# Kernel optimization log

Hardware: AMD Instinct MI355X
Metric: run time of the kernel (lower is better)

The kernel has to match this reference:

```python
import jax, jax.numpy as jnp
import numpy as np

LEFT = 16  # attention window size (previous `left` symbols incl. current)


def _make_history(symbols, left):
    """contexts[b, t, j] = symbols[b, t - (left-1-j)] for j in [0,left),
    padded with symbols[b, 0] for out-of-range positions (pad = symbols[:, :1])."""
    B, T = symbols.shape
    # (T, left) gather index matrix
    idx = jnp.arange(T)[:, None] - (left - 1 - jnp.arange(left))[None, :]
    valid = idx >= 0
    idx_c = jnp.clip(idx, 0, T - 1)
    ctx = symbols[:, idx_c]                                   # (B, T, left)
    pad = symbols[:, :1][:, :, None]                          # (B, 1, 1)
    return jnp.where(valid[None, :, :], ctx, pad)             # (B, T, left)


def setup_inputs() -> dict:
    key = jax.random.key(0)
    k1, k2, k3, k4 = jax.random.split(key, 4)
    B, T, V, D = 8, 2048, 256, 512
    symbols = jax.random.randint(k1, (B, T), 0, V, dtype=jnp.int32)
    encodings = jax.random.normal(k2, (B, T, D), dtype=jnp.float32)
    # keras 'uniform' initializer: U(-0.05, 0.05)
    M = jax.random.uniform(k3, (V, D), minval=-0.05, maxval=0.05, dtype=jnp.float32)
    C = jax.random.uniform(k4, (V, D), minval=-0.05, maxval=0.05, dtype=jnp.float32)
    return {"symbols": symbols, "encodings": encodings, "M": M, "C": C}


def reference(symbols, encodings, M, C):
    contexts = _make_history(symbols, LEFT)                   # (B, T, L) int
    Mg = M[contexts]                                          # (B, T, L, D)
    Cg = C[contexts]                                          # (B, T, L, D)
    scores = jnp.einsum('btld,btd->btl', Mg, encodings)       # (B, T, L)
    p = jax.nn.softmax(scores, axis=-1)                       # (B, T, L)
    compressed = jnp.einsum('btl,btld->btd', p, Cg)           # (B, T, D)
    output = jnp.concatenate([compressed, encodings], axis=-1)  # (B, T, 2D)
    return output, p
```

## Files before the change

kernel.cpp:

```cpp
#include <hip/hip_runtime.h>

#define B_ 8
#define T_ 2048
#define V_ 256
#define D_ 512
#define LEFT_ 16
#define TPW 4
#define NR (TPW + LEFT_ - 1)

__device__ __forceinline__ constexpr int rev6(int x) {
    return (((x >> 0) & 1) << 5) | (((x >> 1) & 1) << 4) | (((x >> 2) & 1) << 3) |
           (((x >> 3) & 1) << 2) | (((x >> 4) & 1) << 1) | (((x >> 5) & 1) << 0);
}

__device__ __forceinline__ float dot8(const float4& m0, const float4& m1,
                                      const float4& e0, const float4& e1) {
    return m0.x * e0.x + m0.y * e0.y + m0.z * e0.z + m0.w * e0.w
         + m1.x * e1.x + m1.y * e1.y + m1.z * e1.z + m1.w * e1.w;
}

__global__ __launch_bounds__(256)
void attn_cell_kernel(const int* __restrict__ symbols,
                      const float* __restrict__ encodings,
                      const float* __restrict__ M,
                      const float* __restrict__ C,
                      float* __restrict__ out,
                      float* __restrict__ p_out) {
    const int tid  = threadIdx.x;
    const int lane = tid & 63;
    const int w    = tid >> 6;

    const int blk = blockIdx.x;
    const int b   = blk >> 7;
    const int tb  = (blk & 127) * 16 + w * TPW;
    const int* symrow = symbols + b * T_;
    const size_t rowbase = (size_t)b * T_ + tb;
    const int dof = lane * 8;

    int syms[NR];
    #pragma unroll
    for (int i = 0; i < NR; ++i) {
        int pos = tb - (LEFT_ - 1) + i;
        pos = max(pos, 0);
        syms[i] = symrow[pos];
    }

    float4 e0[TPW], e1[TPW];
    #pragma unroll
    for (int tk = 0; tk < TPW; ++tk) {
        const float* e = encodings + (rowbase + tk) * D_ + dof;
        e0[tk] = *(const float4*)e;
        e1[tk] = *(const float4*)(e + 4);
    }

    float s[64];
    #pragma unroll
    for (int v = 0; v < 64; ++v) s[v] = 0.f;

    #pragma unroll
    for (int i = 0; i < NR; ++i) {
        const float* mr = M + (size_t)syms[i] * D_ + dof;
        const float4 m0 = *(const float4*)mr;
        const float4 m1 = *(const float4*)(mr + 4);
        #pragma unroll
        for (int tk = 0; tk < TPW; ++tk) {
            const int sl = i - tk;
            if (sl >= 0 && sl < 16)
                s[(tk << 4) | sl] += dot8(m0, m1, e0[tk], e1[tk]);
        }
    }

    #pragma unroll
    for (int k = 0; k < 32; ++k) {
        const float lo = s[k], hi = s[k + 32];
        const float sd = (lane & 1) ? lo : hi;
        const float rv = __shfl_xor(sd, 1);
        s[k] = (lane & 1) ? hi + rv : lo + rv;
    }
    #pragma unroll
    for (int k = 0; k < 16; ++k) {
        const float lo = s[k], hi = s[k + 16];
        const float sd = (lane & 2) ? lo : hi;
        const float rv = __shfl_xor(sd, 2);
        s[k] = (lane & 2) ? hi + rv : lo + rv;
    }
    #pragma unroll
    for (int k = 0; k < 8; ++k) {
        const float lo = s[k], hi = s[k + 8];
        const float sd = (lane & 4) ? lo : hi;
        const float rv = __shfl_xor(sd, 4);
        s[k] = (lane & 4) ? hi + rv : lo + rv;
    }
    #pragma unroll
    for (int k = 0; k < 4; ++k) {
        const float lo = s[k], hi = s[k + 4];
        const float sd = (lane & 8) ? lo : hi;
        const float rv = __shfl_xor(sd, 8);
        s[k] = (lane & 8) ? hi + rv : lo + rv;
    }
    #pragma unroll
    for (int k = 0; k < 2; ++k) {
        const float lo = s[k], hi = s[k + 2];
        const float sd = (lane & 16) ? lo : hi;
        const float rv = __shfl_xor(sd, 16);
        s[k] = (lane & 16) ? hi + rv : lo + rv;
    }
    {
        const float lo = s[0], hi = s[1];
        const float sd = (lane & 32) ? lo : hi;
        const float rv = __shfl_xor(sd, 32);
        s[0] = (lane & 32) ? hi + rv : lo + rv;
    }
    const float v = s[0];

    float mx = v;
    mx = fmaxf(mx, __shfl_xor(mx, 4));
    mx = fmaxf(mx, __shfl_xor(mx, 8));
    mx = fmaxf(mx, __shfl_xor(mx, 16));
    mx = fmaxf(mx, __shfl_xor(mx, 32));
    const float ex = __expf(v - mx);
    float sum = ex;
    sum += __shfl_xor(sum, 4);
    sum += __shfl_xor(sum, 8);
    sum += __shfl_xor(sum, 16);
    sum += __shfl_xor(sum, 32);
    const float p = ex / sum;

    {
        const int idx  = rev6(lane);
        const int tk_o = idx >> 4;
        const int sl_o = idx & 15;
        p_out[(rowbase + tk_o) * 16 + sl_o] = p;
    }

    float4 a0[TPW], a1[TPW];
    #pragma unroll
    for (int tk = 0; tk < TPW; ++tk) {
        a0[tk] = make_float4(0.f, 0.f, 0.f, 0.f);
        a1[tk] = make_float4(0.f, 0.f, 0.f, 0.f);
    }

    #pragma unroll
    for (int i = 0; i < NR; ++i) {
        const float* cr = C + (size_t)syms[i] * D_ + dof;
        const float4 c0 = *(const float4*)cr;
        const float4 c1 = *(const float4*)(cr + 4);
        #pragma unroll
        for (int tk = 0; tk < TPW; ++tk) {
            const int sl = i - tk;
            if (sl >= 0 && sl < 16) {
                const float pb = __shfl(p, rev6((tk << 4) | sl));
                a0[tk].x += pb * c0.x; a0[tk].y += pb * c0.y;
                a0[tk].z += pb * c0.z; a0[tk].w += pb * c0.w;
                a1[tk].x += pb * c1.x; a1[tk].y += pb * c1.y;
                a1[tk].z += pb * c1.z; a1[tk].w += pb * c1.w;
            }
        }
    }

    #pragma unroll
    for (int tk = 0; tk < TPW; ++tk) {
        float* ob = out + (rowbase + tk) * 1024 + dof;
        *(float4*)ob       = a0[tk];
        *(float4*)(ob + 4) = a1[tk];
        *(float4*)(ob + D_)     = e0[tk];
        *(float4*)(ob + D_ + 4) = e1[tk];
    }
}

extern "C" void kernel_launch(void* const* d_in, const int* in_sizes, int n_in,
                              void* d_out, int out_size, void* d_ws, size_t ws_size,
                              hipStream_t stream) {
    const int*   symbols   = (const int*)d_in[0];
    const float* encodings = (const float*)d_in[1];
    const float* M         = (const float*)d_in[2];
    const float* C         = (const float*)d_in[3];
    float* out   = (float*)d_out;
    float* p_out = out + (size_t)B_ * T_ * 1024;

    dim3 grid(B_ * (T_ / 16));
    attn_cell_kernel<<<grid, 256, 0, stream>>>(symbols, encodings, M, C, out, p_out);
}
```

Measured before the change: 33.30 us.

## Process timesteps one at a time per wave with fewer rows per wave

Cuts timesteps per wave from 4 to 2 and processes each timestep in turn with a 16-entry score array instead of a 64-entry one. This lowers register pressure and doubles the grid size, aiming at higher occupancy. Symbol indices are made wave-uniform with readfirstlane so the row addresses can sit in scalar registers. In exchange, M and C rows shared between neighbouring timesteps are reloaded rather than reused in registers, which adds gather traffic through the cache.

```diff
diff --git a/kernel.cpp b/kernel.cpp
--- a/kernel.cpp
+++ b/kernel.cpp
@@ -5,12 +5,12 @@
 #define V_ 256
 #define D_ 512
 #define LEFT_ 16
-#define TPW 4
-#define NR (TPW + LEFT_ - 1)
+#define TPW 2
+#define NRW (TPW + LEFT_ - 1)
 
-__device__ __forceinline__ constexpr int rev6(int x) {
-    return (((x >> 0) & 1) << 5) | (((x >> 1) & 1) << 4) | (((x >> 2) & 1) << 3) |
-           (((x >> 3) & 1) << 2) | (((x >> 4) & 1) << 1) | (((x >> 5) & 1) << 0);
+__device__ __forceinline__ constexpr int rev4(int x) {
+    return (((x >> 0) & 1) << 3) | (((x >> 1) & 1) << 2) |
+           (((x >> 2) & 1) << 1) | (((x >> 3) & 1) << 0);
 }
 
 __device__ __forceinline__ float dot8(const float4& m0, const float4& m1,
@@ -31,140 +31,99 @@
     const int w    = tid >> 6;
 
     const int blk = blockIdx.x;
-    const int b   = blk >> 7;
-    const int tb  = (blk & 127) * 16 + w * TPW;
+    const int b   = blk >> 8;
+    const int tw  = (blk & 255) * (4 * TPW) + w * TPW;
     const int* symrow = symbols + b * T_;
-    const size_t rowbase = (size_t)b * T_ + tb;
+    const size_t rowbase = (size_t)b * T_ + tw;
     const int dof = lane * 8;
 
-    int syms[NR];
+    int syms[NRW];
     #pragma unroll
-    for (int i = 0; i < NR; ++i) {
-        int pos = tb - (LEFT_ - 1) + i;
+    for (int i = 0; i < NRW; ++i) {
+        int pos = tw - (LEFT_ - 1) + i;
         pos = max(pos, 0);
-        syms[i] = symrow[pos];
-    }
-
-    float4 e0[TPW], e1[TPW];
-    #pragma unroll
-    for (int tk = 0; tk < TPW; ++tk) {
-        const float* e = encodings + (rowbase + tk) * D_ + dof;
-        e0[tk] = *(const float4*)e;
-        e1[tk] = *(const float4*)(e + 4);
-    }
-
-    float s[64];
-    #pragma unroll
-    for (int v = 0; v < 64; ++v) s[v] = 0.f;
-
-    #pragma unroll
-    for (int i = 0; i < NR; ++i) {
-        const float* mr = M + (size_t)syms[i] * D_ + dof;
-        const float4 m0 = *(const float4*)mr;
-        const float4 m1 = *(const float4*)(mr + 4);
-        #pragma unroll
-        for (int tk = 0; tk < TPW; ++tk) {
-            const int sl = i - tk;
-            if (sl >= 0 && sl < 16)
-                s[(tk << 4) | sl] += dot8(m0, m1, e0[tk], e1[tk]);
-        }
-    }
-
-    #pragma unroll
-    for (int k = 0; k < 32; ++k) {
-        const float lo = s[k], hi = s[k + 32];
-        const float sd = (lane & 1) ? lo : hi;
-        const float rv = __shfl_xor(sd, 1);
-        s[k] = (lane & 1) ? hi + rv : lo + rv;
-    }
-    #pragma unroll
-    for (int k = 0; k < 16; ++k) {
-        const float lo = s[k], hi = s[k + 16];
-        const float sd = (lane & 2) ? lo : hi;
-        const float rv = __shfl_xor(sd, 2);
-        s[k] = (lane & 2) ? hi + rv : lo + rv;
-    }
-    #pragma unroll
-    for (int k = 0; k < 8; ++k) {
-        const float lo = s[k], hi = s[k + 8];
-        const float sd = (lane & 4) ? lo : hi;
-        const float rv = __shfl_xor(sd, 4);
-        s[k] = (lane & 4) ? hi + rv : lo + rv;
-    }
-    #pragma unroll
-    for (int k = 0; k < 4; ++k) {
-        const float lo = s[k], hi = s[k + 4];
-        const float sd = (lane & 8) ? lo : hi;
-        const float rv = __shfl_xor(sd, 8);
-        s[k] = (lane & 8) ? hi + rv : lo + rv;
-    }
-    #pragma unroll
-    for (int k = 0; k < 2; ++k) {
-        const float lo = s[k], hi = s[k + 2];
-        const float sd = (lane & 16) ? lo : hi;
-        const float rv = __shfl_xor(sd, 16);
-        s[k] = (lane & 16) ? hi + rv : lo + rv;
-    }
-    {
-        const float lo = s[0], hi = s[1];
-        const float sd = (lane & 32) ? lo : hi;
-        const float rv = __shfl_xor(sd, 32);
-        s[0] = (lane & 32) ? hi + rv : lo + rv;
-    }
-    const float v = s[0];
-
-    float mx = v;
-    mx = fmaxf(mx, __shfl_xor(mx, 4));
-    mx = fmaxf(mx, __shfl_xor(mx, 8));
-    mx = fmaxf(mx, __shfl_xor(mx, 16));
-    mx = fmaxf(mx, __shfl_xor(mx, 32));
-    const float ex = __expf(v - mx);
-    float sum = ex;
-    sum += __shfl_xor(sum, 4);
-    sum += __shfl_xor(sum, 8);
-    sum += __shfl_xor(sum, 16);
-    sum += __shfl_xor(sum, 32);
-    const float p = ex / sum;
-
-    {
-        const int idx  = rev6(lane);
-        const int tk_o = idx >> 4;
-        const int sl_o = idx & 15;
-        p_out[(rowbase + tk_o) * 16 + sl_o] = p;
-    }
-
-    float4 a0[TPW], a1[TPW];
-    #pragma unroll
-    for (int tk = 0; tk < TPW; ++tk) {
-        a0[tk] = make_float4(0.f, 0.f, 0.f, 0.f);
-        a1[tk] = make_float4(0.f, 0.f, 0.f, 0.f);
-    }
-
-    #pragma unroll
-    for (int i = 0; i < NR; ++i) {
-        const float* cr = C + (size_t)syms[i] * D_ + dof;
-        const float4 c0 = *(const float4*)cr;
-        const float4 c1 = *(const float4*)(cr + 4);
-        #pragma unroll
-        for (int tk = 0; tk < TPW; ++tk) {
-            const int sl = i - tk;
-            if (sl >= 0 && sl < 16) {
-                const float pb = __shfl(p, rev6((tk << 4) | sl));
-                a0[tk].x += pb * c0.x; a0[tk].y += pb * c0.y;
-                a0[tk].z += pb * c0.z; a0[tk].w += pb * c0.w;
-                a1[tk].x += pb * c1.x; a1[tk].y += pb * c1.y;
-                a1[tk].z += pb * c1.z; a1[tk].w += pb * c1.w;
-            }
-        }
+        syms[i] = __builtin_amdgcn_readfirstlane(symrow[pos]);
     }
 
     #pragma unroll
     for (int tk = 0; tk < TPW; ++tk) {
+        const float* e = encodings + (rowbase + tk) * D_ + dof;
+        const float4 e0 = *(const float4*)e;
+        const float4 e1 = *(const float4*)(e + 4);
+
+        float s[16];
+        #pragma unroll
+        for (int l = 0; l < 16; ++l) {
+            const float* mr = M + (size_t)syms[tk + l] * D_ + dof;
+            const float4 m0 = *(const float4*)mr;
+            const float4 m1 = *(const float4*)(mr + 4);
+            s[l] = dot8(m0, m1, e0, e1);
+        }
+
+        #pragma unroll
+        for (int k = 0; k < 8; ++k) {
+            const float lo = s[k], hi = s[k + 8];
+            const float sd = (lane & 1) ? lo : hi;
+            const float rv = __shfl_xor(sd, 1);
+            s[k] = (lane & 1) ? hi + rv : lo + rv;
+        }
+        #pragma unroll
+        for (int k = 0; k < 4; ++k) {
+            const float lo = s[k], hi = s[k + 4];
+            const float sd = (lane & 2) ? lo : hi;
+            const float rv = __shfl_xor(sd, 2);
+            s[k] = (lane & 2) ? hi + rv : lo + rv;
+        }
+        #pragma unroll
+        for (int k = 0; k < 2; ++k) {
+            const float lo = s[k], hi = s[k + 2];
+            const float sd = (lane & 4) ? lo : hi;
+            const float rv = __shfl_xor(sd, 4);
+            s[k] = (lane & 4) ? hi + rv : lo + rv;
+        }
+        {
+            const float lo = s[0], hi = s[1];
+            const float sd = (lane & 8) ? lo : hi;
+            const float rv = __shfl_xor(sd, 8);
+            s[0] = (lane & 8) ? hi + rv : lo + rv;
+        }
+        float v = s[0];
+        v += __shfl_xor(v, 16);
+        v += __shfl_xor(v, 32);
+
+        float mx = v;
+        mx = fmaxf(mx, __shfl_xor(mx, 1));
+        mx = fmaxf(mx, __shfl_xor(mx, 2));
+        mx = fmaxf(mx, __shfl_xor(mx, 4));
+        mx = fmaxf(mx, __shfl_xor(mx, 8));
+        const float ex = __expf(v - mx);
+        float sum = ex;
+        sum += __shfl_xor(sum, 1);
+        sum += __shfl_xor(sum, 2);
+        sum += __shfl_xor(sum, 4);
+        sum += __shfl_xor(sum, 8);
+        const float p = ex / sum;
+
+        if (lane < 16)
+            p_out[(rowbase + tk) * 16 + rev4(lane)] = p;
+
+        float4 a0 = make_float4(0.f, 0.f, 0.f, 0.f);
+        float4 a1 = make_float4(0.f, 0.f, 0.f, 0.f);
+        #pragma unroll
+        for (int l = 0; l < 16; ++l) {
+            const float* cr = C + (size_t)syms[tk + l] * D_ + dof;
+            const float4 c0 = *(const float4*)cr;
+            const float4 c1 = *(const float4*)(cr + 4);
+            const float pb = __shfl(p, rev4(l));
+            a0.x += pb * c0.x; a0.y += pb * c0.y; a0.z += pb * c0.z; a0.w += pb * c0.w;
+            a1.x += pb * c1.x; a1.y += pb * c1.y; a1.z += pb * c1.z; a1.w += pb * c1.w;
+        }
+
         float* ob = out + (rowbase + tk) * 1024 + dof;
-        *(float4*)ob       = a0[tk];
-        *(float4*)(ob + 4) = a1[tk];
-        *(float4*)(ob + D_)     = e0[tk];
-        *(float4*)(ob + D_ + 4) = e1[tk];
+        *(float4*)ob            = a0;
+        *(float4*)(ob + 4)      = a1;
+        *(float4*)(ob + D_)     = e0;
+        *(float4*)(ob + D_ + 4) = e1;
     }
 }
 
@@ -178,6 +137,6 @@
     float* out   = (float*)d_out;
     float* p_out = out + (size_t)B_ * T_ * 1024;
 
-    dim3 grid(B_ * (T_ / 16));
+    dim3 grid(B_ * (T_ / (4 * TPW)));
     attn_cell_kernel<<<grid, 256, 0, stream>>>(symbols, encodings, M, C, out, p_out);
 }
```

Result: slower. 56.12 us (+68.6%).
